# Performance work log

Hardware: AMD Instinct MI355X
Metric: run time of the kernel (lower is better)

## Reference

```python
import jax, jax.numpy as jnp
import numpy as np

IN_F = 4096
OUT_F = 4096
SPLIT_F = 410   # ceil(4096 * 0.1)
NUM_PARTS = 10  # ceil(4096 / 410)


def setup_inputs() -> dict:
    key = jax.random.key(0)
    ks = jax.random.split(key, 7)
    s = 1.0 / np.sqrt(IN_F)
    sn = 1.0 / np.sqrt(NUM_PARTS)
    return {
        'x': jax.random.normal(ks[0], (2, 2048, IN_F), dtype=jnp.float32),
        'Wsel': jax.random.uniform(ks[1], (NUM_PARTS, IN_F), jnp.float32, -s, s),
        'bsel': jax.random.uniform(ks[2], (NUM_PARTS,), jnp.float32, -s, s),
        'Wexp': jax.random.uniform(ks[3], (IN_F, NUM_PARTS), jnp.float32, -sn, sn),
        'bexp': jax.random.uniform(ks[4], (IN_F,), jnp.float32, -sn, sn),
        'Wfc': jax.random.uniform(ks[5], (SPLIT_F, IN_F), jnp.float32, -s, s),
        'bfc': jax.random.uniform(ks[6], (SPLIT_F,), jnp.float32, -s, s),
        'out_features': OUT_F,
    }


def reference(x, Wsel, bsel, Wexp, bexp, Wfc, bfc, out_features):
    # selector: sx[..., n]
    sx = jnp.einsum('bsi,ni->bsn', x, Wsel) + bsel
    # expander(diag_embed(sx)): px[..., n, f] = sx[..., n] * Wexp[f, n] + bexp[f]
    # (diag matrix never materialized; mathematically identical)
    px = sx[..., :, None] * Wexp.T[None, None, :, :] + bexp  # [b, s, n, in]
    xx = x[..., None, :] + px                                # broadcast-add of x
    y = jnp.einsum('bsni,fi->bsnf', xx, Wfc) + bfc           # splitfc, [b, s, n, sf]
    y = y.reshape(y.shape[0], y.shape[1], -1)                # (n sf) flatten
    return y[..., :out_features]
```

## Files before the change

kernel.cpp:

```cpp
#include <hip/hip_runtime.h>
#include <hip/hip_bf16.h>
#include <stdint.h>

#define TKS    4096
#define KD     4096
#define NSF    410
#define NPARTS 10
#define OUTF   4096

typedef unsigned short u16;
typedef __attribute__((ext_vector_type(8))) short bf16x8;
typedef __attribute__((ext_vector_type(4))) float f32x4;

#define WS_XB  0
#define WS_BSW ((size_t)TKS * KD * 2)
#define WS_SX  (WS_BSW + (size_t)448 * 512 * 8 * 2)
#define WS_GC  (WS_SX + (size_t)TKS * NPARTS * 4)
#define WS_WSL (WS_BSW + (size_t)512 * KD * 2)
#define WS_WEX (WS_WSL + (size_t)16 * KD * 2)

__device__ inline u16 f2bf(float f) {
    union { __hip_bfloat16 b; u16 u; } cv;
    cv.b = __float2bfloat16(f);
    return cv.u;
}

__device__ inline int g_row(int g) { int s = g >> 6; return (s >> 2) * 32 + (s & 1) * 16 + (g & 15); }
__device__ inline int g_col(int g) { int s = g >> 6; return ((s >> 1) & 1) * 32 + ((g >> 4) & 3) * 8; }

__global__ __launch_bounds__(256) void prep_w(const float* __restrict__ Wsel,
                                              const float* __restrict__ Wexp,
                                              const float* __restrict__ bexp,
                                              u16* __restrict__ wselb,
                                              u16* __restrict__ wexpb) {
    const int kt = blockIdx.x;
    const int tid = threadIdx.x;
    const int g  = tid & 127;
    const int ml = g & 15;
    const int col = kt * 64 + (g >> 6) * 32 + ((g >> 4) & 3) * 8;
    u16 h[8];
    if (tid < 128) {
#pragma unroll
        for (int j = 0; j < 8; ++j)
            h[j] = (ml < NPARTS) ? f2bf(Wsel[(size_t)ml * KD + col + j]) : (u16)0;
        *(uint4*)&wselb[((size_t)kt * 128 + g) * 8] = *(uint4*)h;
    } else {
#pragma unroll
        for (int j = 0; j < 8; ++j)
            h[j] = (ml < NPARTS) ? f2bf(Wexp[(size_t)(col + j) * NPARTS + ml])
                 : (ml == NPARTS ? f2bf(bexp[col + j]) : (u16)0);
        *(uint4*)&wexpb[((size_t)kt * 128 + g) * 8] = *(uint4*)h;
    }
}

__global__ __launch_bounds__(256) void retile_b(const float* __restrict__ Wfc,
                                                u16* __restrict__ bsw) {
    const int kt = blockIdx.x & 63, rb = blockIdx.x >> 6;
    const int tid = threadIdx.x;
    u16* tout = bsw + ((size_t)(rb * 64 + kt) * 512) * 8;
#pragma unroll
    for (int j = 0; j < 2; ++j) {
        const int g = j * 256 + tid;
        const int r = rb * 64 + g_row(g);
        uint4 pk = make_uint4(0u, 0u, 0u, 0u);
        if (r < NSF) {
            const float* src = Wfc + (size_t)r * KD + kt * 64 + g_col(g);
            float4 v0 = *(const float4*)src;
            float4 v1 = *(const float4*)(src + 4);
            u16 h[8] = { f2bf(v0.x), f2bf(v0.y), f2bf(v0.z), f2bf(v0.w),
                         f2bf(v1.x), f2bf(v1.y), f2bf(v1.z), f2bf(v1.w) };
            pk = *(uint4*)h;
        }
        *(uint4*)&tout[(size_t)g * 8] = pk;
    }
}

__global__ __launch_bounds__(256) void retile_x(const float* __restrict__ x,
                                                u16* __restrict__ xb) {
    const int kt = blockIdx.x & 63, tb = blockIdx.x >> 6;
    const int g = threadIdx.x;
    const int slot = g >> 6;
    const int row = (slot & 1) * 16 + (g & 15);
    const int col = (slot >> 1) * 32 + ((g >> 4) & 3) * 8;
    const float* src = x + (size_t)(tb * 32 + row) * KD + kt * 64 + col;
    float4 v0 = *(const float4*)src;
    float4 v1 = *(const float4*)(src + 4);
    u16 h[8] = { f2bf(v0.x), f2bf(v0.y), f2bf(v0.z), f2bf(v0.w),
                 f2bf(v1.x), f2bf(v1.y), f2bf(v1.z), f2bf(v1.w) };
    *(uint4*)&xb[((size_t)(tb * 64 + kt) * 256 + g) * 8] = *(uint4*)h;
}

__global__ __launch_bounds__(256) void sel_g(const u16* __restrict__ xb,
                                             const u16* __restrict__ bsw,
                                             const u16* __restrict__ wselb,
                                             const u16* __restrict__ wexpb,
                                             const float* __restrict__ bsel,
                                             const float* __restrict__ bfc,
                                             float* __restrict__ sxb,
                                             float* __restrict__ gc) {
    __shared__ float lred[4][64][16];
    const int tid = threadIdx.x, lane = tid & 63, w = tid >> 6;
    const int q = lane >> 4, ml = lane & 15;
    const int b = blockIdx.x;

    if (b < 128) {
        f32x4 a0 = (f32x4){0.f,0.f,0.f,0.f}, a1 = (f32x4){0.f,0.f,0.f,0.f};
        for (int kt = w * 16; kt < w * 16 + 16; ++kt) {
#pragma unroll
            for (int ks = 0; ks < 2; ++ks) {
                bf16x8 wl  = *(const bf16x8*)&wselb[((size_t)kt * 128 + ks * 64 + lane) * 8];
                bf16x8 av0 = *(const bf16x8*)&xb[(((size_t)b * 64 + kt) * 256 + (ks * 2 + 0) * 64 + lane) * 8];
                bf16x8 av1 = *(const bf16x8*)&xb[(((size_t)b * 64 + kt) * 256 + (ks * 2 + 1) * 64 + lane) * 8];
                a0 = __builtin_amdgcn_mfma_f32_16x16x32_bf16(av0, wl, a0, 0, 0, 0);
                a1 = __builtin_amdgcn_mfma_f32_16x16x32_bf16(av1, wl, a1, 0, 0, 0);
            }
        }
#pragma unroll
        for (int r = 0; r < 4; ++r) {
            lred[w][q * 4 + r][ml]      = a0[r];
            lred[w][16 + q * 4 + r][ml] = a1[r];
        }
        __syncthreads();
        for (int i = tid; i < 32 * NPARTS; i += 256) {
            const int t = i / NPARTS, n = i % NPARTS;
            sxb[((size_t)b * 32 + t) * NPARTS + n] =
                lred[0][t][n] + lred[1][t][n] + lred[2][t][n] + lred[3][t][n] + bsel[n];
        }
    } else {
        const int fb = b - 128;
        f32x4 g0 = (f32x4){0.f,0.f,0.f,0.f}, g1 = g0, g2 = g0, g3 = g0;
        for (int kt = w * 16; kt < w * 16 + 16; ++kt) {
#pragma unroll
            for (int ks = 0; ks < 2; ++ks) {
                bf16x8 ef = *(const bf16x8*)&wexpb[((size_t)kt * 128 + ks * 64 + lane) * 8];
                bf16x8 b0 = *(const bf16x8*)&bsw[(((size_t)fb * 64 + kt) * 512 + (0 * 4 + ks * 2 + 0) * 64 + lane) * 8];
                bf16x8 b1 = *(const bf16x8*)&bsw[(((size_t)fb * 64 + kt) * 512 + (0 * 4 + ks * 2 + 1) * 64 + lane) * 8];
                bf16x8 b2 = *(const bf16x8*)&bsw[(((size_t)fb * 64 + kt) * 512 + (1 * 4 + ks * 2 + 0) * 64 + lane) * 8];
                bf16x8 b3 = *(const bf16x8*)&bsw[(((size_t)fb * 64 + kt) * 512 + (1 * 4 + ks * 2 + 1) * 64 + lane) * 8];
                g0 = __builtin_amdgcn_mfma_f32_16x16x32_bf16(b0, ef, g0, 0, 0, 0);
                g1 = __builtin_amdgcn_mfma_f32_16x16x32_bf16(b1, ef, g1, 0, 0, 0);
                g2 = __builtin_amdgcn_mfma_f32_16x16x32_bf16(b2, ef, g2, 0, 0, 0);
                g3 = __builtin_amdgcn_mfma_f32_16x16x32_bf16(b3, ef, g3, 0, 0, 0);
            }
        }
#pragma unroll
        for (int r = 0; r < 4; ++r) {
            lred[w][ 0 + q * 4 + r][ml] = g0[r];
            lred[w][16 + q * 4 + r][ml] = g1[r];
            lred[w][32 + q * 4 + r][ml] = g2[r];
            lred[w][48 + q * 4 + r][ml] = g3[r];
        }
        __syncthreads();
        for (int i = tid; i < 64 * 11; i += 256) {
            const int f = i / 11, c = i % 11;
            float s = lred[0][f][c] + lred[1][f][c] + lred[2][f][c] + lred[3][f][c];
            const int fg = fb * 64 + f;
            if (c == 10) s += (fg < NSF ? bfc[fg] : 0.f);
            gc[(size_t)fg * 12 + c] = s;
        }
    }
}

#define A_IDX(kt, mi, ks) ((((size_t)(tb * 2 + ((mi) >> 1)) * 64 + (size_t)(kt)) * 256 \
                            + ((ks) * 2 + ((mi) & 1)) * 64 + lane) * 8)
#define B_IDX(kt, nj, ks) (((size_t)(fb * 64 + (kt)) * 512 \
                            + (wf * 4 + (ks) * 2 + (nj)) * 64 + lane) * 8)

__global__ __launch_bounds__(256, 4) void main_kernel(const u16* __restrict__ xb,
                                                      const u16* __restrict__ bsw,
                                                      const float* __restrict__ sxb,
                                                      const float* __restrict__ gc,
                                                      float* __restrict__ out) {
    __shared__ float red[4][4][16][34];
    __shared__ float sxt[64][NPARTS];
    __shared__ float gt[32][12];

    const int tid = threadIdx.x;
    const int f2 = blockIdx.x >> 6;
    const int tb = blockIdx.x & 63;
    const int lane = tid & 63;
    const int kh = tid >> 6;
    const int q = lane >> 4, ml = lane & 15;
    const int fb = f2 >> 1, wf = f2 & 1;

    f32x4 acc[4][2];
#pragma unroll
    for (int mi = 0; mi < 4; ++mi)
#pragma unroll
        for (int nj = 0; nj < 2; ++nj) acc[mi][nj] = (f32x4){0.f,0.f,0.f,0.f};

    bf16x8 fa[2][4], fbv[2][2];

#define LOADAB(p, kt, ks) do {                                            \
        _Pragma("unroll")                                                 \
        for (int mi = 0; mi < 4; ++mi)                                    \
            fa[p][mi] = *(const bf16x8*)&xb[A_IDX((kt), mi, (ks))];       \
        _Pragma("unroll")                                                 \
        for (int nj = 0; nj < 2; ++nj)                                    \
            fbv[p][nj] = *(const bf16x8*)&bsw[B_IDX((kt), nj, (ks))];     \
    } while (0)

#define MFMAS(p) do {                                                     \
        _Pragma("unroll")                                                 \
        for (int mi = 0; mi < 4; ++mi)                                    \
            _Pragma("unroll")                                             \
            for (int nj = 0; nj < 2; ++nj)                                \
                acc[mi][nj] = __builtin_amdgcn_mfma_f32_16x16x32_bf16(    \
                    fa[p][mi], fbv[p][nj], acc[mi][nj], 0, 0, 0);         \
    } while (0)

    LOADAB(0, kh * 16, 0);
    for (int it2 = 0; it2 < 16; ++it2) {
        const int kt = kh * 16 + it2;
        LOADAB(1, kt, 1);
        MFMAS(0);
        if (it2 + 1 < 16) LOADAB(0, kt + 1, 0);
        MFMAS(1);
    }
#undef LOADAB
#undef MFMAS

#pragma unroll
    for (int mi = 0; mi < 4; ++mi)
#pragma unroll
        for (int nj = 0; nj < 2; ++nj)
#pragma unroll
            for (int r = 0; r < 4; ++r)
                red[mi][kh][q * 4 + r][nj * 16 + ml] = acc[mi][nj][r];

    for (int i = tid; i < 64 * NPARTS; i += 256)
        sxt[i / NPARTS][i % NPARTS] = sxb[((size_t)tb * 64 + i / NPARTS) * NPARTS + i % NPARTS];
    for (int i = tid; i < 32 * 11; i += 256)
        gt[i / 11][i % 11] = gc[((size_t)f2 * 32 + i / 11) * 12 + i % 11];
    __syncthreads();

#pragma unroll
    for (int nj = 0; nj < 2; ++nj) {
        const int fl = nj * 16 + ml;
        const int fg = f2 * 32 + fl;
        if (fg >= NSF) continue;
        const float cv = gt[fl][10];
        float gv[NPARTS];
#pragma unroll
        for (int n = 0; n < NPARTS; ++n) gv[n] = gt[fl][n];
#pragma unroll
        for (int r = 0; r < 4; ++r) {
            const int tl = kh * 16 + q * 4 + r;
            const float v = red[kh][0][q * 4 + r][fl] + red[kh][1][q * 4 + r][fl]
                          + red[kh][2][q * 4 + r][fl] + red[kh][3][q * 4 + r][fl];
            const float av = v + cv;
            float* orow = out + (size_t)(tb * 64 + tl) * OUTF;
#pragma unroll
            for (int n = 0; n < NPARTS; ++n) {
                const int j = n * NSF + fg;
                if (j < OUTF) orow[j] = av + sxt[tl][n] * gv[n];
            }
        }
    }
}

extern "C" void kernel_launch(void* const* d_in, const int* in_sizes, int n_in,
                              void* d_out, int out_size, void* d_ws, size_t ws_size,
                              hipStream_t stream) {
    const float* x    = (const float*)d_in[0];
    const float* Wsel = (const float*)d_in[1];
    const float* bsel = (const float*)d_in[2];
    const float* Wexp = (const float*)d_in[3];
    const float* bexp = (const float*)d_in[4];
    const float* Wfc  = (const float*)d_in[5];
    const float* bfc  = (const float*)d_in[6];
    float* out = (float*)d_out;

    char* ws = (char*)d_ws;
    u16* xb    = (u16*)(ws + WS_XB);
    u16* bsw   = (u16*)(ws + WS_BSW);
    u16* wselb = (u16*)(ws + WS_WSL);
    u16* wexpb = (u16*)(ws + WS_WEX);
    float* sxb = (float*)(ws + WS_SX);
    float* gcv = (float*)(ws + WS_GC);

    prep_w<<<dim3(64), dim3(256), 0, stream>>>(Wsel, Wexp, bexp, wselb, wexpb);
    retile_b<<<dim3(7 * 64), dim3(256), 0, stream>>>(Wfc, bsw);
    retile_x<<<dim3(128 * 64), dim3(256), 0, stream>>>(x, xb);
    sel_g<<<dim3(135), dim3(256), 0, stream>>>(xb, bsw, wselb, wexpb, bsel, bfc, sxb, gcv);
    main_kernel<<<dim3(13 * 64), dim3(256), 0, stream>>>(xb, bsw, sxb, gcv, out);
}
```

Baseline: 215.7 us.

## Fuse preprocessing kernels into one launch with fp32 selector math and deeper prefetch

Merges the weight prep, Wfc retile, x retile and selector/gc kernels into a single prep kernel. The selector projection and the Wfc·Wexp products are now computed directly in fp32 from the original inputs with wave reductions, rather than through bf16 MFMA over retiled data. This removes three launches and the serial dependency between them. The main kernel's software pipeline goes from a 2-stage to a 4-stage register prefetch, and its occupancy hint in launch_bounds is dropped. The risks are higher register pressure in the main kernel and slow FMA-bound fp32 blocks in prep that may end up on the critical path.

```diff
diff --git a/kernel.cpp b/kernel.cpp
--- a/kernel.cpp
+++ b/kernel.cpp
@@ -16,8 +16,6 @@
 #define WS_BSW ((size_t)TKS * KD * 2)
 #define WS_SX  (WS_BSW + (size_t)448 * 512 * 8 * 2)
 #define WS_GC  (WS_SX + (size_t)TKS * NPARTS * 4)
-#define WS_WSL (WS_BSW + (size_t)512 * KD * 2)
-#define WS_WEX (WS_WSL + (size_t)16 * KD * 2)
 
 __device__ inline u16 f2bf(float f) {
     union { __hip_bfloat16 b; u16 u; } cv;
@@ -28,135 +26,140 @@
 __device__ inline int g_row(int g) { int s = g >> 6; return (s >> 2) * 32 + (s & 1) * 16 + (g & 15); }
 __device__ inline int g_col(int g) { int s = g >> 6; return ((s >> 1) & 1) * 32 + ((g >> 4) & 3) * 8; }
 
-__global__ __launch_bounds__(256) void prep_w(const float* __restrict__ Wsel,
-                                              const float* __restrict__ Wexp,
-                                              const float* __restrict__ bexp,
-                                              u16* __restrict__ wselb,
-                                              u16* __restrict__ wexpb) {
-    const int kt = blockIdx.x;
+__global__ __launch_bounds__(256) void prep(const float* __restrict__ x,
+                                            const float* __restrict__ Wsel,
+                                            const float* __restrict__ bsel,
+                                            const float* __restrict__ Wexp,
+                                            const float* __restrict__ bexp,
+                                            const float* __restrict__ Wfc,
+                                            const float* __restrict__ bfc,
+                                            u16* __restrict__ xb,
+                                            u16* __restrict__ bsw,
+                                            float* __restrict__ sxb,
+                                            float* __restrict__ gc) {
+    const int bid = blockIdx.x;
     const int tid = threadIdx.x;
-    const int g  = tid & 127;
-    const int ml = g & 15;
-    const int col = kt * 64 + (g >> 6) * 32 + ((g >> 4) & 3) * 8;
-    u16 h[8];
-    if (tid < 128) {
-#pragma unroll
-        for (int j = 0; j < 8; ++j)
-            h[j] = (ml < NPARTS) ? f2bf(Wsel[(size_t)ml * KD + col + j]) : (u16)0;
-        *(uint4*)&wselb[((size_t)kt * 128 + g) * 8] = *(uint4*)h;
+
+    if (bid < 8192) {
+        const int kt = bid & 63, tb = bid >> 6;
+        const int g = tid;
+        const int slot = g >> 6;
+        const int row = (slot & 1) * 16 + (g & 15);
+        const int col = (slot >> 1) * 32 + ((g >> 4) & 3) * 8;
+        const float* src = x + (size_t)(tb * 32 + row) * KD + kt * 64 + col;
+        float4 v0 = *(const float4*)src;
+        float4 v1 = *(const float4*)(src + 4);
+        u16 h[8] = { f2bf(v0.x), f2bf(v0.y), f2bf(v0.z), f2bf(v0.w),
+                     f2bf(v1.x), f2bf(v1.y), f2bf(v1.z), f2bf(v1.w) };
+        *(uint4*)&xb[((size_t)(tb * 64 + kt) * 256 + g) * 8] = *(uint4*)h;
+
+    } else if (bid < 8640) {
+        const int b2 = bid - 8192;
+        const int kt = b2 & 63, rb = b2 >> 6;
+        u16* tout = bsw + ((size_t)(rb * 64 + kt) * 512) * 8;
+#pragma unroll
+        for (int j = 0; j < 2; ++j) {
+            const int g = j * 256 + tid;
+            const int r = rb * 64 + g_row(g);
+            uint4 pk = make_uint4(0u, 0u, 0u, 0u);
+            if (r < NSF) {
+                const float* src = Wfc + (size_t)r * KD + kt * 64 + g_col(g);
+                float4 v0 = *(const float4*)src;
+                float4 v1 = *(const float4*)(src + 4);
+                u16 h[8] = { f2bf(v0.x), f2bf(v0.y), f2bf(v0.z), f2bf(v0.w),
+                             f2bf(v1.x), f2bf(v1.y), f2bf(v1.z), f2bf(v1.w) };
+                pk = *(uint4*)h;
+            }
+            *(uint4*)&tout[(size_t)g * 8] = pk;
+        }
+
+    } else if (bid < 8768) {
+        const int b3 = bid - 8640;
+        const int w = tid >> 6, lane = tid & 63;
+        const int t0 = b3 * 32 + w * 8;
+        float acc[8][NPARTS];
+#pragma unroll
+        for (int t = 0; t < 8; ++t)
+#pragma unroll
+            for (int n = 0; n < NPARTS; ++n) acc[t][n] = 0.f;
+
+        for (int k4 = 0; k4 < 16; ++k4) {
+            const int k = k4 * 256 + lane * 4;
+            float4 ws[NPARTS];
+#pragma unroll
+            for (int n = 0; n < NPARTS; ++n)
+                ws[n] = *(const float4*)&Wsel[(size_t)n * KD + k];
+#pragma unroll
+            for (int t = 0; t < 8; ++t) {
+                float4 xv = *(const float4*)&x[(size_t)(t0 + t) * KD + k];
+#pragma unroll
+                for (int n = 0; n < NPARTS; ++n)
+                    acc[t][n] += xv.x * ws[n].x + xv.y * ws[n].y
+                               + xv.z * ws[n].z + xv.w * ws[n].w;
+            }
+        }
+#pragma unroll
+        for (int s = 1; s < 64; s <<= 1)
+#pragma unroll
+            for (int t = 0; t < 8; ++t)
+#pragma unroll
+                for (int n = 0; n < NPARTS; ++n)
+                    acc[t][n] += __shfl_xor(acc[t][n], s);
+        if (lane == 0) {
+#pragma unroll
+            for (int t = 0; t < 8; ++t)
+#pragma unroll
+                for (int n = 0; n < NPARTS; ++n)
+                    sxb[(size_t)(t0 + t) * NPARTS + n] = acc[t][n] + bsel[n];
+        }
+
     } else {
-#pragma unroll
-        for (int j = 0; j < 8; ++j)
-            h[j] = (ml < NPARTS) ? f2bf(Wexp[(size_t)(col + j) * NPARTS + ml])
-                 : (ml == NPARTS ? f2bf(bexp[col + j]) : (u16)0);
-        *(uint4*)&wexpb[((size_t)kt * 128 + g) * 8] = *(uint4*)h;
-    }
-}
-
-__global__ __launch_bounds__(256) void retile_b(const float* __restrict__ Wfc,
-                                                u16* __restrict__ bsw) {
-    const int kt = blockIdx.x & 63, rb = blockIdx.x >> 6;
-    const int tid = threadIdx.x;
-    u16* tout = bsw + ((size_t)(rb * 64 + kt) * 512) * 8;
-#pragma unroll
-    for (int j = 0; j < 2; ++j) {
-        const int g = j * 256 + tid;
-        const int r = rb * 64 + g_row(g);
-        uint4 pk = make_uint4(0u, 0u, 0u, 0u);
-        if (r < NSF) {
-            const float* src = Wfc + (size_t)r * KD + kt * 64 + g_col(g);
-            float4 v0 = *(const float4*)src;
-            float4 v1 = *(const float4*)(src + 4);
-            u16 h[8] = { f2bf(v0.x), f2bf(v0.y), f2bf(v0.z), f2bf(v0.w),
-                         f2bf(v1.x), f2bf(v1.y), f2bf(v1.z), f2bf(v1.w) };
-            pk = *(uint4*)h;
-        }
-        *(uint4*)&tout[(size_t)g * 8] = pk;
-    }
-}
-
-__global__ __launch_bounds__(256) void retile_x(const float* __restrict__ x,
-                                                u16* __restrict__ xb) {
-    const int kt = blockIdx.x & 63, tb = blockIdx.x >> 6;
-    const int g = threadIdx.x;
-    const int slot = g >> 6;
-    const int row = (slot & 1) * 16 + (g & 15);
-    const int col = (slot >> 1) * 32 + ((g >> 4) & 3) * 8;
-    const float* src = x + (size_t)(tb * 32 + row) * KD + kt * 64 + col;
-    float4 v0 = *(const float4*)src;
-    float4 v1 = *(const float4*)(src + 4);
-    u16 h[8] = { f2bf(v0.x), f2bf(v0.y), f2bf(v0.z), f2bf(v0.w),
-                 f2bf(v1.x), f2bf(v1.y), f2bf(v1.z), f2bf(v1.w) };
-    *(uint4*)&xb[((size_t)(tb * 64 + kt) * 256 + g) * 8] = *(uint4*)h;
-}
-
-__global__ __launch_bounds__(256) void sel_g(const u16* __restrict__ xb,
-                                             const u16* __restrict__ bsw,
-                                             const u16* __restrict__ wselb,
-                                             const u16* __restrict__ wexpb,
-                                             const float* __restrict__ bsel,
-                                             const float* __restrict__ bfc,
-                                             float* __restrict__ sxb,
-                                             float* __restrict__ gc) {
-    __shared__ float lred[4][64][16];
-    const int tid = threadIdx.x, lane = tid & 63, w = tid >> 6;
-    const int q = lane >> 4, ml = lane & 15;
-    const int b = blockIdx.x;
-
-    if (b < 128) {
-        f32x4 a0 = (f32x4){0.f,0.f,0.f,0.f}, a1 = (f32x4){0.f,0.f,0.f,0.f};
-        for (int kt = w * 16; kt < w * 16 + 16; ++kt) {
-#pragma unroll
-            for (int ks = 0; ks < 2; ++ks) {
-                bf16x8 wl  = *(const bf16x8*)&wselb[((size_t)kt * 128 + ks * 64 + lane) * 8];
-                bf16x8 av0 = *(const bf16x8*)&xb[(((size_t)b * 64 + kt) * 256 + (ks * 2 + 0) * 64 + lane) * 8];
-                bf16x8 av1 = *(const bf16x8*)&xb[(((size_t)b * 64 + kt) * 256 + (ks * 2 + 1) * 64 + lane) * 8];
-                a0 = __builtin_amdgcn_mfma_f32_16x16x32_bf16(av0, wl, a0, 0, 0, 0);
-                a1 = __builtin_amdgcn_mfma_f32_16x16x32_bf16(av1, wl, a1, 0, 0, 0);
-            }
-        }
-#pragma unroll
-        for (int r = 0; r < 4; ++r) {
-            lred[w][q * 4 + r][ml]      = a0[r];
-            lred[w][16 + q * 4 + r][ml] = a1[r];
-        }
-        __syncthreads();
-        for (int i = tid; i < 32 * NPARTS; i += 256) {
-            const int t = i / NPARTS, n = i % NPARTS;
-            sxb[((size_t)b * 32 + t) * NPARTS + n] =
-                lred[0][t][n] + lred[1][t][n] + lred[2][t][n] + lred[3][t][n] + bsel[n];
-        }
-    } else {
-        const int fb = b - 128;
-        f32x4 g0 = (f32x4){0.f,0.f,0.f,0.f}, g1 = g0, g2 = g0, g3 = g0;
-        for (int kt = w * 16; kt < w * 16 + 16; ++kt) {
-#pragma unroll
-            for (int ks = 0; ks < 2; ++ks) {
-                bf16x8 ef = *(const bf16x8*)&wexpb[((size_t)kt * 128 + ks * 64 + lane) * 8];
-                bf16x8 b0 = *(const bf16x8*)&bsw[(((size_t)fb * 64 + kt) * 512 + (0 * 4 + ks * 2 + 0) * 64 + lane) * 8];
-                bf16x8 b1 = *(const bf16x8*)&bsw[(((size_t)fb * 64 + kt) * 512 + (0 * 4 + ks * 2 + 1) * 64 + lane) * 8];
-                bf16x8 b2 = *(const bf16x8*)&bsw[(((size_t)fb * 64 + kt) * 512 + (1 * 4 + ks * 2 + 0) * 64 + lane) * 8];
-                bf16x8 b3 = *(const bf16x8*)&bsw[(((size_t)fb * 64 + kt) * 512 + (1 * 4 + ks * 2 + 1) * 64 + lane) * 8];
-                g0 = __builtin_amdgcn_mfma_f32_16x16x32_bf16(b0, ef, g0, 0, 0, 0);
-                g1 = __builtin_amdgcn_mfma_f32_16x16x32_bf16(b1, ef, g1, 0, 0, 0);
-                g2 = __builtin_amdgcn_mfma_f32_16x16x32_bf16(b2, ef, g2, 0, 0, 0);
-                g3 = __builtin_amdgcn_mfma_f32_16x16x32_bf16(b3, ef, g3, 0, 0, 0);
-            }
-        }
-#pragma unroll
-        for (int r = 0; r < 4; ++r) {
-            lred[w][ 0 + q * 4 + r][ml] = g0[r];
-            lred[w][16 + q * 4 + r][ml] = g1[r];
-            lred[w][32 + q * 4 + r][ml] = g2[r];
-            lred[w][48 + q * 4 + r][ml] = g3[r];
-        }
-        __syncthreads();
-        for (int i = tid; i < 64 * 11; i += 256) {
-            const int f = i / 11, c = i % 11;
-            float s = lred[0][f][c] + lred[1][f][c] + lred[2][f][c] + lred[3][f][c];
-            const int fg = fb * 64 + f;
-            if (c == 10) s += (fg < NSF ? bfc[fg] : 0.f);
-            gc[(size_t)fg * 12 + c] = s;
+        const int b4 = bid - 8768;
+        const int w = tid >> 6, lane = tid & 63;
+        const int f0 = b4 * 32 + w * 8;
+        float acc[8][11];
+#pragma unroll
+        for (int t = 0; t < 8; ++t)
+#pragma unroll
+            for (int n = 0; n < 11; ++n) acc[t][n] = 0.f;
+
+        for (int k4 = 0; k4 < 16; ++k4) {
+            const int k = k4 * 256 + lane * 4;
+            float we[4][11];
+#pragma unroll
+            for (int j = 0; j < 4; ++j) {
+#pragma unroll
+                for (int n = 0; n < NPARTS; ++n)
+                    we[j][n] = Wexp[(size_t)(k + j) * NPARTS + n];
+                we[j][10] = bexp[k + j];
+            }
+#pragma unroll
+            for (int t = 0; t < 8; ++t) {
+                const int f = f0 + t;
+                float4 xv = (f < NSF) ? *(const float4*)&Wfc[(size_t)f * KD + k]
+                                      : make_float4(0.f, 0.f, 0.f, 0.f);
+#pragma unroll
+                for (int n = 0; n < 11; ++n)
+                    acc[t][n] += xv.x * we[0][n] + xv.y * we[1][n]
+                               + xv.z * we[2][n] + xv.w * we[3][n];
+            }
+        }
+#pragma unroll
+        for (int s = 1; s < 64; s <<= 1)
+#pragma unroll
+            for (int t = 0; t < 8; ++t)
+#pragma unroll
+                for (int n = 0; n < 11; ++n)
+                    acc[t][n] += __shfl_xor(acc[t][n], s);
+        if (lane == 0) {
+#pragma unroll
+            for (int t = 0; t < 8; ++t) {
+                const int f = f0 + t;
+#pragma unroll
+                for (int n = 0; n < NPARTS; ++n)
+                    gc[(size_t)f * 12 + n] = (f < NSF) ? acc[t][n] : 0.f;
+                gc[(size_t)f * 12 + 10] = (f < NSF) ? acc[t][10] + bfc[f] : 0.f;
+            }
         }
     }
 }
@@ -166,11 +169,11 @@
 #define B_IDX(kt, nj, ks) (((size_t)(fb * 64 + (kt)) * 512 \
                             + (wf * 4 + (ks) * 2 + (nj)) * 64 + lane) * 8)
 
-__global__ __launch_bounds__(256, 4) void main_kernel(const u16* __restrict__ xb,
-                                                      const u16* __restrict__ bsw,
-                                                      const float* __restrict__ sxb,
-                                                      const float* __restrict__ gc,
-                                                      float* __restrict__ out) {
+__global__ __launch_bounds__(256) void main_kernel(const u16* __restrict__ xb,
+                                                   const u16* __restrict__ bsw,
+                                                   const float* __restrict__ sxb,
+                                                   const float* __restrict__ gc,
+                                                   float* __restrict__ out) {
     __shared__ float red[4][4][16][34];
     __shared__ float sxt[64][NPARTS];
     __shared__ float gt[32][12];
@@ -189,7 +192,7 @@
 #pragma unroll
         for (int nj = 0; nj < 2; ++nj) acc[mi][nj] = (f32x4){0.f,0.f,0.f,0.f};
 
-    bf16x8 fa[2][4], fbv[2][2];
+    bf16x8 fa[4][4], fbv[4][2];
 
 #define LOADAB(p, kt, ks) do {                                            \
         _Pragma("unroll")                                                 \
@@ -209,14 +212,15 @@
                     fa[p][mi], fbv[p][nj], acc[mi][nj], 0, 0, 0);         \
     } while (0)
 
-    LOADAB(0, kh * 16, 0);
-    for (int it2 = 0; it2 < 16; ++it2) {
-        const int kt = kh * 16 + it2;
-        LOADAB(1, kt, 1);
-        MFMAS(0);
-        if (it2 + 1 < 16) LOADAB(0, kt + 1, 0);
-        MFMAS(1);
+#define LD(p, s) LOADAB((p), kh * 16 + ((s) >> 1), (s) & 1)
+
+    LD(0, 0); LD(1, 1); LD(2, 2);
+#pragma unroll
+    for (int s = 0; s < 32; ++s) {
+        if (s + 3 < 32) LD((s + 3) & 3, s + 3);
+        MFMAS(s & 3);
     }
+#undef LD
 #undef LOADAB
 #undef MFMAS
 
@@ -274,14 +278,10 @@
     char* ws = (char*)d_ws;
     u16* xb    = (u16*)(ws + WS_XB);
     u16* bsw   = (u16*)(ws + WS_BSW);
-    u16* wselb = (u16*)(ws + WS_WSL);
-    u16* wexpb = (u16*)(ws + WS_WEX);
     float* sxb = (float*)(ws + WS_SX);
     float* gcv = (float*)(ws + WS_GC);
 
-    prep_w<<<dim3(64), dim3(256), 0, stream>>>(Wsel, Wexp, bexp, wselb, wexpb);
-    retile_b<<<dim3(7 * 64), dim3(256), 0, stream>>>(Wfc, bsw);
-    retile_x<<<dim3(128 * 64), dim3(256), 0, stream>>>(x, xb);
-    sel_g<<<dim3(135), dim3(256), 0, stream>>>(xb, bsw, wselb, wexpb, bsel, bfc, sxb, gcv);
+    prep<<<dim3(8192 + 448 + 128 + 14), dim3(256), 0, stream>>>(
+        x, Wsel, bsel, Wexp, bexp, Wfc, bfc, xb, bsw, sxb, gcv);
     main_kernel<<<dim3(13 * 64), dim3(256), 0, stream>>>(xb, bsw, sxb, gcv, out);
 }
```

Result: slower. 227.6 us (+5.5%).
